# Kernel optimization log

Measured on AMD Instinct MI355X. Metric: run time of the kernel, lower is better.

The kernel has to match this reference:

```python
import jax, jax.numpy as jnp
import numpy as np

N = 50000      # nodes
E = 800000     # edges (avg degree 16)
D_IN = 128     # in_feats
D_H = 128      # n_hidden
D_OUT = 64     # n_classes


def _lin(k, fan_in, fan_out):
    # torch nn.Linear default init: U(-1/sqrt(fan_in), 1/sqrt(fan_in))
    s = 1.0 / np.sqrt(fan_in)
    return jax.random.uniform(k, (fan_in, fan_out), jnp.float32, -s, s)


def setup_inputs() -> dict:
    key = jax.random.key(0)
    ks = jax.random.split(key, 12)
    return {
        "x": jax.random.normal(ks[0], (N, D_IN), jnp.float32),
        "edge_src": jax.random.randint(ks[1], (E,), 0, N, jnp.int32),
        "edge_dst": jax.random.randint(ks[2], (E,), 0, N, jnp.int32),
        # layer 0: in_feats -> n_hidden
        "W_self0": _lin(ks[3], D_IN, D_H),
        "W_neigh0": _lin(ks[4], D_IN, D_H),
        "b0": jnp.zeros((D_H,), jnp.float32),
        # layer 1: n_hidden -> n_hidden
        "W_self1": _lin(ks[5], D_H, D_H),
        "W_neigh1": _lin(ks[6], D_H, D_H),
        "b1": jnp.zeros((D_H,), jnp.float32),
        # layer 2: n_hidden -> n_classes
        "W_self2": _lin(ks[7], D_H, D_OUT),
        "W_neigh2": _lin(ks[8], D_H, D_OUT),
        "b2": jnp.zeros((D_OUT,), jnp.float32),
    }


def _sage_conv(x, src, dst, W_self, W_neigh, b):
    """DGL SAGEConv with 'mean' aggregator:
    out = x @ W_self + mean_{u in N(v)} x_u @ W_neigh + b
    Zero in-degree nodes get zero neighbor term (degree clamped to 1)."""
    n = x.shape[0]
    agg = jax.ops.segment_sum(x[src], dst, num_segments=n)          # [N, d]
    deg = jax.ops.segment_sum(jnp.ones((src.shape[0],), x.dtype), dst,
                              num_segments=n)                        # [N]
    h_neigh = agg / jnp.maximum(deg, 1.0)[:, None]
    return x @ W_self + h_neigh @ W_neigh + b


def reference(x, edge_src, edge_dst,
              W_self0, W_neigh0, b0,
              W_self1, W_neigh1, b1,
              W_self2, W_neigh2, b2):
    # dropout is identity in eval/inference mode
    h = jax.nn.relu(_sage_conv(x, edge_src, edge_dst, W_self0, W_neigh0, b0))
    h = jax.nn.relu(_sage_conv(h, edge_src, edge_dst, W_self1, W_neigh1, b1))
    return _sage_conv(h, edge_src, edge_dst, W_self2, W_neigh2, b2)
```

## Files before the change

kernel.cpp:

```cpp
#include <hip/hip_runtime.h>

#define NN 50000
#define NPAD 50048
#define NE 800000
#define CAP 64
#define NSLICE 6250

#define EBG 391
#define EDGE_BLOCKS (EBG * 8)
#define CVT_BLOCKS 782
#define W_BLOCKS 320
#define PREP_GRID (EDGE_BLOCKS + CVT_BLOCKS + W_BLOCKS)

typedef _Float16 f16;
typedef _Float16 f16x8 __attribute__((ext_vector_type(8)));
typedef float f32x4 __attribute__((ext_vector_type(4)));

__global__ __launch_bounds__(256) void prep_kernel(
    const float* __restrict__ X, const int* __restrict__ esrc,
    const int* __restrict__ edst,
    const float* __restrict__ WS0, const float* __restrict__ WN0,
    const float* __restrict__ WS1, const float* __restrict__ WN1,
    const float* __restrict__ WS2, const float* __restrict__ WN2,
    f16* __restrict__ XH, f16* __restrict__ wt0, f16* __restrict__ wt1,
    f16* __restrict__ wt2, int* __restrict__ cursor, int* __restrict__ eidx) {
    const int bid = blockIdx.x;
    if (bid < EDGE_BLOCKS) {
        const int g = bid & 7;
        const int gi = bid >> 3;
        const int lo = g * NSLICE, hi = lo + NSLICE;
        const int per = (NE + EBG - 1) / EBG;
        const int s = gi * per;
        const int e_end = (s + per < NE) ? s + per : NE;
        for (int e = s + threadIdx.x; e < e_end; e += 256) {
            int d = edst[e];
            if (d >= lo && d < hi) {
                int p = atomicAdd(&cursor[d], 1);
                if (p < CAP) eidx[(d << 6) + p] = esrc[e];
            }
        }
    } else if (bid < EDGE_BLOCKS + CVT_BLOCKS) {
        const int total8 = NN * 128 / 8;
        int t = (bid - EDGE_BLOCKS) * 256 + threadIdx.x;
        for (int i = t; i < total8; i += CVT_BLOCKS * 256) {
            float4 v0 = *reinterpret_cast<const float4*>(X + (size_t)i * 8);
            float4 v1 = *reinterpret_cast<const float4*>(X + (size_t)i * 8 + 4);
            f16x8 o = {(f16)v0.x, (f16)v0.y, (f16)v0.z, (f16)v0.w,
                       (f16)v1.x, (f16)v1.y, (f16)v1.z, (f16)v1.w};
            *reinterpret_cast<f16x8*>(XH + (size_t)i * 8) = o;
        }
    } else {
        int t = (bid - EDGE_BLOCKS - CVT_BLOCKS) * 256 + threadIdx.x;
        if (t < 32768) {
            int j = t >> 8, k = t & 255;
            float v = (k < 128) ? WS0[k * 128 + j] : WN0[(k - 128) * 128 + j];
            wt0[j * 256 + k] = (f16)v;
        } else if (t < 65536) {
            int u = t - 32768;
            int j = u >> 8, k = u & 255;
            float v = (k < 128) ? WS1[k * 128 + j] : WN1[(k - 128) * 128 + j];
            wt1[j * 256 + k] = (f16)v;
        } else if (t < 81920) {
            int u = t - 65536;
            int j = u >> 7, k = u & 127;
            float v = (j < 64) ? WS2[k * 64 + j] : WN2[k * 64 + (j - 64)];
            wt2[j * 128 + k] = (f16)v;
        }
    }
}

__global__ __launch_bounds__(256) void gather_mean4(const f16* __restrict__ X,
                                                    const int* __restrict__ cnt_,
                                                    const int* __restrict__ eidx,
                                                    f16* __restrict__ OUT, int n) {
    int wave = blockIdx.x * 4 + (threadIdx.x >> 6);
    int lane = threadIdx.x & 63;
    int node = wave * 4 + (lane >> 4);
    int sl = lane & 15;
    if (node >= n) return;
    int cnt = cnt_[node];
    const int* row = eidx + ((size_t)node << 6);
    float acc[8];
#pragma unroll
    for (int j = 0; j < 8; j++) acc[j] = 0.f;
    int e = 0;
    for (; e + 8 <= cnt; e += 8) {
        int4 sa = *reinterpret_cast<const int4*>(row + e);
        int4 sb = *reinterpret_cast<const int4*>(row + e + 4);
        f16x8 v0 = *reinterpret_cast<const f16x8*>(X + (size_t)sa.x * 128 + sl * 8);
        f16x8 v1 = *reinterpret_cast<const f16x8*>(X + (size_t)sa.y * 128 + sl * 8);
        f16x8 v2 = *reinterpret_cast<const f16x8*>(X + (size_t)sa.z * 128 + sl * 8);
        f16x8 v3 = *reinterpret_cast<const f16x8*>(X + (size_t)sa.w * 128 + sl * 8);
        f16x8 v4 = *reinterpret_cast<const f16x8*>(X + (size_t)sb.x * 128 + sl * 8);
        f16x8 v5 = *reinterpret_cast<const f16x8*>(X + (size_t)sb.y * 128 + sl * 8);
        f16x8 v6 = *reinterpret_cast<const f16x8*>(X + (size_t)sb.z * 128 + sl * 8);
        f16x8 v7 = *reinterpret_cast<const f16x8*>(X + (size_t)sb.w * 128 + sl * 8);
#pragma unroll
        for (int j = 0; j < 8; j++)
            acc[j] += (((float)v0[j] + (float)v1[j]) + ((float)v2[j] + (float)v3[j])) +
                      (((float)v4[j] + (float)v5[j]) + ((float)v6[j] + (float)v7[j]));
    }
    for (; e + 4 <= cnt; e += 4) {
        int4 s4 = *reinterpret_cast<const int4*>(row + e);
        f16x8 v0 = *reinterpret_cast<const f16x8*>(X + (size_t)s4.x * 128 + sl * 8);
        f16x8 v1 = *reinterpret_cast<const f16x8*>(X + (size_t)s4.y * 128 + sl * 8);
        f16x8 v2 = *reinterpret_cast<const f16x8*>(X + (size_t)s4.z * 128 + sl * 8);
        f16x8 v3 = *reinterpret_cast<const f16x8*>(X + (size_t)s4.w * 128 + sl * 8);
#pragma unroll
        for (int j = 0; j < 8; j++)
            acc[j] += ((float)v0[j] + (float)v1[j]) + ((float)v2[j] + (float)v3[j]);
    }
    for (; e < cnt; e++) {
        int s0 = row[e];
        f16x8 v0 = *reinterpret_cast<const f16x8*>(X + (size_t)s0 * 128 + sl * 8);
#pragma unroll
        for (int j = 0; j < 8; j++) acc[j] += (float)v0[j];
    }
    float iv = 1.0f / fmaxf((float)cnt, 1.0f);
    f16x8 o;
#pragma unroll
    for (int j = 0; j < 8; j++) o[j] = (f16)(acc[j] * iv);
    *reinterpret_cast<f16x8*>(OUT + (size_t)node * 128 + sl * 8) = o;
}

__global__ __launch_bounds__(256) void gather_out(const f16* __restrict__ Y,
                                                  const int* __restrict__ cnt_,
                                                  const int* __restrict__ eidx,
                                                  float* __restrict__ OUT, int n) {
    int wave = blockIdx.x * 4 + (threadIdx.x >> 6);
    int lane = threadIdx.x & 63;
    int node = wave * 8 + (lane >> 3);
    int sl = lane & 7;
    if (node >= n) return;
    int cnt = cnt_[node];
    const int* row = eidx + ((size_t)node << 6);
    float acc[8];
#pragma unroll
    for (int j = 0; j < 8; j++) acc[j] = 0.f;
    int e = 0;
    for (; e + 8 <= cnt; e += 8) {
        int4 sa = *reinterpret_cast<const int4*>(row + e);
        int4 sb = *reinterpret_cast<const int4*>(row + e + 4);
        f16x8 v0 = *reinterpret_cast<const f16x8*>(Y + (size_t)sa.x * 128 + 64 + sl * 8);
        f16x8 v1 = *reinterpret_cast<const f16x8*>(Y + (size_t)sa.y * 128 + 64 + sl * 8);
        f16x8 v2 = *reinterpret_cast<const f16x8*>(Y + (size_t)sa.z * 128 + 64 + sl * 8);
        f16x8 v3 = *reinterpret_cast<const f16x8*>(Y + (size_t)sa.w * 128 + 64 + sl * 8);
        f16x8 v4 = *reinterpret_cast<const f16x8*>(Y + (size_t)sb.x * 128 + 64 + sl * 8);
        f16x8 v5 = *reinterpret_cast<const f16x8*>(Y + (size_t)sb.y * 128 + 64 + sl * 8);
        f16x8 v6 = *reinterpret_cast<const f16x8*>(Y + (size_t)sb.z * 128 + 64 + sl * 8);
        f16x8 v7 = *reinterpret_cast<const f16x8*>(Y + (size_t)sb.w * 128 + 64 + sl * 8);
#pragma unroll
        for (int j = 0; j < 8; j++)
            acc[j] += (((float)v0[j] + (float)v1[j]) + ((float)v2[j] + (float)v3[j])) +
                      (((float)v4[j] + (float)v5[j]) + ((float)v6[j] + (float)v7[j]));
    }
    for (; e + 4 <= cnt; e += 4) {
        int4 s4 = *reinterpret_cast<const int4*>(row + e);
        f16x8 v0 = *reinterpret_cast<const f16x8*>(Y + (size_t)s4.x * 128 + 64 + sl * 8);
        f16x8 v1 = *reinterpret_cast<const f16x8*>(Y + (size_t)s4.y * 128 + 64 + sl * 8);
        f16x8 v2 = *reinterpret_cast<const f16x8*>(Y + (size_t)s4.z * 128 + 64 + sl * 8);
        f16x8 v3 = *reinterpret_cast<const f16x8*>(Y + (size_t)s4.w * 128 + 64 + sl * 8);
#pragma unroll
        for (int j = 0; j < 8; j++)
            acc[j] += ((float)v0[j] + (float)v1[j]) + ((float)v2[j] + (float)v3[j]);
    }
    for (; e < cnt; e++) {
        int s0 = row[e];
        f16x8 v0 = *reinterpret_cast<const f16x8*>(Y + (size_t)s0 * 128 + 64 + sl * 8);
#pragma unroll
        for (int j = 0; j < 8; j++) acc[j] += (float)v0[j];
    }
    float iv = 1.0f / fmaxf((float)cnt, 1.0f);
    f16x8 self = *reinterpret_cast<const f16x8*>(Y + (size_t)node * 128 + sl * 8);
    float o[8];
#pragma unroll
    for (int j = 0; j < 8; j++) o[j] = acc[j] * iv + (float)self[j];
    float* dst = OUT + (size_t)node * 64 + sl * 8;
    *reinterpret_cast<float4*>(dst) = *reinterpret_cast<float4*>(o);
    *reinterpret_cast<float4*>(dst + 4) = *reinterpret_cast<float4*>(o + 4);
}

template <int DOUT, int K, bool RELU, bool HALFBIAS>
__global__ __launch_bounds__(256) void mfma_gemm(const f16* __restrict__ A1,
                                                 const f16* __restrict__ A2,
                                                 const f16* __restrict__ WT,
                                                 const float* __restrict__ BIAS,
                                                 f16* __restrict__ O16, int n) {
    constexpr int MT = 4;
    constexpr int NT = 4;
    const int lane = threadIdx.x & 63;
    const int wid = threadIdx.x >> 6;
    const int m0 = blockIdx.x * 128 + (wid >> 1) * 64;
    const int n0 = (wid & 1) * 64;

    const int ar = lane & 15;
    const int kg = (lane >> 4) * 8;

    f32x4 acc[MT][NT];
#pragma unroll
    for (int mt = 0; mt < MT; mt++)
#pragma unroll
        for (int nt = 0; nt < NT; nt++) acc[mt][nt] = (f32x4){0.f, 0.f, 0.f, 0.f};

#pragma unroll
    for (int k0 = 0; k0 < K; k0 += 32) {
        const f16* Abase = (K == 256 && k0 >= 128) ? A2 : A1;
        const int kk = (k0 & 127) + kg;
        f16x8 a[MT], b[NT];
#pragma unroll
        for (int mt = 0; mt < MT; mt++)
            a[mt] = *reinterpret_cast<const f16x8*>(
                Abase + (size_t)(m0 + mt * 16 + ar) * 128 + kk);
#pragma unroll
        for (int nt = 0; nt < NT; nt++)
            b[nt] = *reinterpret_cast<const f16x8*>(
                WT + (size_t)(n0 + nt * 16 + ar) * K + k0 + kg);
#pragma unroll
        for (int mt = 0; mt < MT; mt++)
#pragma unroll
            for (int nt = 0; nt < NT; nt++)
                acc[mt][nt] = __builtin_amdgcn_mfma_f32_16x16x32_f16(
                    a[mt], b[nt], acc[mt][nt], 0, 0, 0);
    }

    const int orow = (lane >> 4) * 4;
    const int ocol = lane & 15;
#pragma unroll
    for (int nt = 0; nt < NT; nt++) {
        const int col = n0 + nt * 16 + ocol;
        const float bias = HALFBIAS ? (col < 64 ? BIAS[col] : 0.f) : BIAS[col];
#pragma unroll
        for (int mt = 0; mt < MT; mt++) {
#pragma unroll
            for (int j = 0; j < 4; j++) {
                int row = m0 + mt * 16 + orow + j;
                if (row < n) {
                    float v = acc[mt][nt][j] + bias;
                    if (RELU) v = fmaxf(v, 0.f);
                    O16[(size_t)row * DOUT + col] = (f16)v;
                }
            }
        }
    }
}

extern "C" void kernel_launch(void* const* d_in, const int* in_sizes, int n_in,
                              void* d_out, int out_size, void* d_ws, size_t ws_size,
                              hipStream_t stream) {
    const float* x        = (const float*)d_in[0];
    const int*   esrc     = (const int*)d_in[1];
    const int*   edst     = (const int*)d_in[2];
    const float* W_self0  = (const float*)d_in[3];
    const float* W_neigh0 = (const float*)d_in[4];
    const float* b0       = (const float*)d_in[5];
    const float* W_self1  = (const float*)d_in[6];
    const float* W_neigh1 = (const float*)d_in[7];
    const float* b1       = (const float*)d_in[8];
    const float* W_self2  = (const float*)d_in[9];
    const float* W_neigh2 = (const float*)d_in[10];
    const float* b2       = (const float*)d_in[11];
    float* out = (float*)d_out;

    char* ws = (char*)d_ws;
    auto align1k = [](size_t v) { return (v + 1023) & ~(size_t)1023; };
    size_t off = 0;
    int* cursor = (int*)(ws + off); off = align1k(off + (size_t)NN * 4);
    int* eidx   = (int*)(ws + off); off = align1k(off + (size_t)NN * CAP * 4);
    f16* wt0    = (f16*)(ws + off); off = align1k(off + (size_t)128 * 256 * 2);
    f16* wt1    = (f16*)(ws + off); off = align1k(off + (size_t)128 * 256 * 2);
    f16* wt2    = (f16*)(ws + off); off = align1k(off + (size_t)128 * 128 * 2);
    const size_t FEAT16 = (size_t)NPAD * 128 * 2;
    f16* xh = (f16*)(ws + off); off += FEAT16;
    f16* hm = (f16*)(ws + off); off += FEAT16;
    f16* h0 = (f16*)(ws + off); off += FEAT16;
    f16* h1 = (f16*)(ws + off); off += FEAT16;

    const int n = NN;
    const int g4blocks = (n + 15) / 16;
    const int g8blocks = (n + 31) / 32;
    const int gemm_blocks = NPAD / 128;

    hipMemsetAsync(cursor, 0, (size_t)n * sizeof(int), stream);
    prep_kernel<<<PREP_GRID, 256, 0, stream>>>(x, esrc, edst,
                                               W_self0, W_neigh0, W_self1, W_neigh1,
                                               W_self2, W_neigh2,
                                               xh, wt0, wt1, wt2, cursor, eidx);

    gather_mean4<<<g4blocks, 256, 0, stream>>>(xh, cursor, eidx, hm, n);
    mfma_gemm<128, 256, true, false><<<gemm_blocks, 256, 0, stream>>>(xh, hm, wt0, b0,
                                                                      h0, n);
    gather_mean4<<<g4blocks, 256, 0, stream>>>(h0, cursor, eidx, hm, n);
    mfma_gemm<128, 256, true, false><<<gemm_blocks, 256, 0, stream>>>(h0, hm, wt1, b1,
                                                                      h1, n);
    mfma_gemm<128, 128, false, true><<<gemm_blocks, 256, 0, stream>>>(h1, nullptr, wt2,
                                                                      b2, hm, n);
    gather_out<<<g8blocks, 256, 0, stream>>>(hm, cursor, eidx, out, n);
}
```

Before: 194.7 us.

## Fuse neighbor gather with GEMM per layer and shrink edge indices to 16-bit

Each hidden layer now gathers and averages neighbor rows into a swizzled LDS tile, then runs the MFMA GEMM from that tile in the same kernel. This removes the global round trip of the mean buffer and one launch per layer. Edge source indices are stored as u16, halving index traffic, but they only fit because N is 50000, below 65536. The degree clamp to CAP is now explicit, and the fused blocks are only 391 blocks of 512 threads, which may limit gather parallelism.

```diff
diff --git a/kernel.cpp b/kernel.cpp
--- a/kernel.cpp
+++ b/kernel.cpp
@@ -15,6 +15,9 @@
 typedef _Float16 f16;
 typedef _Float16 f16x8 __attribute__((ext_vector_type(8)));
 typedef float f32x4 __attribute__((ext_vector_type(4)));
+typedef unsigned short u16;
+typedef unsigned short u16x4 __attribute__((ext_vector_type(4)));
+typedef unsigned short u16x8 __attribute__((ext_vector_type(8)));
 
 __global__ __launch_bounds__(256) void prep_kernel(
     const float* __restrict__ X, const int* __restrict__ esrc,
@@ -23,7 +26,7 @@
     const float* __restrict__ WS1, const float* __restrict__ WN1,
     const float* __restrict__ WS2, const float* __restrict__ WN2,
     f16* __restrict__ XH, f16* __restrict__ wt0, f16* __restrict__ wt1,
-    f16* __restrict__ wt2, int* __restrict__ cursor, int* __restrict__ eidx) {
+    f16* __restrict__ wt2, int* __restrict__ cursor, u16* __restrict__ eidx) {
     const int bid = blockIdx.x;
     if (bid < EDGE_BLOCKS) {
         const int g = bid & 7;
@@ -36,7 +39,7 @@
             int d = edst[e];
             if (d >= lo && d < hi) {
                 int p = atomicAdd(&cursor[d], 1);
-                if (p < CAP) eidx[(d << 6) + p] = esrc[e];
+                if (p < CAP) eidx[(d << 6) + p] = (u16)esrc[e];
             }
         }
     } else if (bid < EDGE_BLOCKS + CVT_BLOCKS) {
@@ -69,97 +72,226 @@
     }
 }
 
-__global__ __launch_bounds__(256) void gather_mean4(const f16* __restrict__ X,
-                                                    const int* __restrict__ cnt_,
-                                                    const int* __restrict__ eidx,
-                                                    f16* __restrict__ OUT, int n) {
-    int wave = blockIdx.x * 4 + (threadIdx.x >> 6);
-    int lane = threadIdx.x & 63;
-    int node = wave * 4 + (lane >> 4);
-    int sl = lane & 15;
-    if (node >= n) return;
-    int cnt = cnt_[node];
-    const int* row = eidx + ((size_t)node << 6);
-    float acc[8];
-#pragma unroll
-    for (int j = 0; j < 8; j++) acc[j] = 0.f;
-    int e = 0;
-    for (; e + 8 <= cnt; e += 8) {
-        int4 sa = *reinterpret_cast<const int4*>(row + e);
-        int4 sb = *reinterpret_cast<const int4*>(row + e + 4);
-        f16x8 v0 = *reinterpret_cast<const f16x8*>(X + (size_t)sa.x * 128 + sl * 8);
-        f16x8 v1 = *reinterpret_cast<const f16x8*>(X + (size_t)sa.y * 128 + sl * 8);
-        f16x8 v2 = *reinterpret_cast<const f16x8*>(X + (size_t)sa.z * 128 + sl * 8);
-        f16x8 v3 = *reinterpret_cast<const f16x8*>(X + (size_t)sa.w * 128 + sl * 8);
-        f16x8 v4 = *reinterpret_cast<const f16x8*>(X + (size_t)sb.x * 128 + sl * 8);
-        f16x8 v5 = *reinterpret_cast<const f16x8*>(X + (size_t)sb.y * 128 + sl * 8);
-        f16x8 v6 = *reinterpret_cast<const f16x8*>(X + (size_t)sb.z * 128 + sl * 8);
-        f16x8 v7 = *reinterpret_cast<const f16x8*>(X + (size_t)sb.w * 128 + sl * 8);
-#pragma unroll
-        for (int j = 0; j < 8; j++)
-            acc[j] += (((float)v0[j] + (float)v1[j]) + ((float)v2[j] + (float)v3[j])) +
-                      (((float)v4[j] + (float)v5[j]) + ((float)v6[j] + (float)v7[j]));
-    }
-    for (; e + 4 <= cnt; e += 4) {
-        int4 s4 = *reinterpret_cast<const int4*>(row + e);
-        f16x8 v0 = *reinterpret_cast<const f16x8*>(X + (size_t)s4.x * 128 + sl * 8);
-        f16x8 v1 = *reinterpret_cast<const f16x8*>(X + (size_t)s4.y * 128 + sl * 8);
-        f16x8 v2 = *reinterpret_cast<const f16x8*>(X + (size_t)s4.z * 128 + sl * 8);
-        f16x8 v3 = *reinterpret_cast<const f16x8*>(X + (size_t)s4.w * 128 + sl * 8);
-#pragma unroll
-        for (int j = 0; j < 8; j++)
-            acc[j] += ((float)v0[j] + (float)v1[j]) + ((float)v2[j] + (float)v3[j]);
-    }
-    for (; e < cnt; e++) {
-        int s0 = row[e];
-        f16x8 v0 = *reinterpret_cast<const f16x8*>(X + (size_t)s0 * 128 + sl * 8);
-#pragma unroll
-        for (int j = 0; j < 8; j++) acc[j] += (float)v0[j];
-    }
-    float iv = 1.0f / fmaxf((float)cnt, 1.0f);
-    f16x8 o;
-#pragma unroll
-    for (int j = 0; j < 8; j++) o[j] = (f16)(acc[j] * iv);
-    *reinterpret_cast<f16x8*>(OUT + (size_t)node * 128 + sl * 8) = o;
+__global__ __launch_bounds__(512) void fused_layer(const f16* __restrict__ X,
+                                                   const int* __restrict__ cnt_,
+                                                   const u16* __restrict__ eidx,
+                                                   const f16* __restrict__ WT,
+                                                   const float* __restrict__ BIAS,
+                                                   f16* __restrict__ O16, int n) {
+    __shared__ f16 hmt[128 * 128];
+    const int lane = threadIdx.x & 63;
+    const int wid = threadIdx.x >> 6;
+    const int rowbase = blockIdx.x * 128;
+
+    {
+        const int sl = lane & 15;
+#pragma unroll 2
+        for (int it = 0; it < 4; it++) {
+            int nl = wid * 16 + it * 4 + (lane >> 4);
+            int node = rowbase + nl;
+            float acc[8];
+#pragma unroll
+            for (int j = 0; j < 8; j++) acc[j] = 0.f;
+            int cdeg = 0;
+            if (node < n) {
+                cdeg = cnt_[node];
+                int cnt = cdeg < CAP ? cdeg : CAP;
+                const u16* row = eidx + ((size_t)node << 6);
+                int e = 0;
+                for (; e + 8 <= cnt; e += 8) {
+                    u16x8 s8 = *reinterpret_cast<const u16x8*>(row + e);
+                    f16x8 v0 = *reinterpret_cast<const f16x8*>(X + (size_t)s8[0] * 128 + sl * 8);
+                    f16x8 v1 = *reinterpret_cast<const f16x8*>(X + (size_t)s8[1] * 128 + sl * 8);
+                    f16x8 v2 = *reinterpret_cast<const f16x8*>(X + (size_t)s8[2] * 128 + sl * 8);
+                    f16x8 v3 = *reinterpret_cast<const f16x8*>(X + (size_t)s8[3] * 128 + sl * 8);
+                    f16x8 v4 = *reinterpret_cast<const f16x8*>(X + (size_t)s8[4] * 128 + sl * 8);
+                    f16x8 v5 = *reinterpret_cast<const f16x8*>(X + (size_t)s8[5] * 128 + sl * 8);
+                    f16x8 v6 = *reinterpret_cast<const f16x8*>(X + (size_t)s8[6] * 128 + sl * 8);
+                    f16x8 v7 = *reinterpret_cast<const f16x8*>(X + (size_t)s8[7] * 128 + sl * 8);
+#pragma unroll
+                    for (int j = 0; j < 8; j++)
+                        acc[j] += (((float)v0[j] + (float)v1[j]) + ((float)v2[j] + (float)v3[j])) +
+                                  (((float)v4[j] + (float)v5[j]) + ((float)v6[j] + (float)v7[j]));
+                }
+                for (; e + 4 <= cnt; e += 4) {
+                    u16x4 s4 = *reinterpret_cast<const u16x4*>(row + e);
+                    f16x8 v0 = *reinterpret_cast<const f16x8*>(X + (size_t)s4[0] * 128 + sl * 8);
+                    f16x8 v1 = *reinterpret_cast<const f16x8*>(X + (size_t)s4[1] * 128 + sl * 8);
+                    f16x8 v2 = *reinterpret_cast<const f16x8*>(X + (size_t)s4[2] * 128 + sl * 8);
+                    f16x8 v3 = *reinterpret_cast<const f16x8*>(X + (size_t)s4[3] * 128 + sl * 8);
+#pragma unroll
+                    for (int j = 0; j < 8; j++)
+                        acc[j] += ((float)v0[j] + (float)v1[j]) + ((float)v2[j] + (float)v3[j]);
+                }
+                for (; e < cnt; e++) {
+                    int s0 = row[e];
+                    f16x8 v0 = *reinterpret_cast<const f16x8*>(X + (size_t)s0 * 128 + sl * 8);
+#pragma unroll
+                    for (int j = 0; j < 8; j++) acc[j] += (float)v0[j];
+                }
+            }
+            float iv = 1.0f / fmaxf((float)cdeg, 1.0f);
+            f16x8 o;
+#pragma unroll
+            for (int j = 0; j < 8; j++) o[j] = (f16)(acc[j] * iv);
+            int chunk = sl ^ (nl & 7);
+            *reinterpret_cast<f16x8*>(hmt + nl * 128 + chunk * 8) = o;
+        }
+    }
+    __syncthreads();
+
+    constexpr int MT = 4, NT = 2;
+    const int rh = wid >> 2;
+    const int n0 = (wid & 3) * 32;
+    const int ar = lane & 15;
+    const int kq = lane >> 4;
+    const int kg = kq * 8;
+
+    f32x4 acc[MT][NT];
+#pragma unroll
+    for (int mt = 0; mt < MT; mt++)
+#pragma unroll
+        for (int nt = 0; nt < NT; nt++) acc[mt][nt] = (f32x4){0.f, 0.f, 0.f, 0.f};
+
+#pragma unroll
+    for (int k0 = 0; k0 < 256; k0 += 32) {
+        f16x8 a[MT], b[NT];
+#pragma unroll
+        for (int mt = 0; mt < MT; mt++) {
+            const int rl = rh * 64 + mt * 16 + ar;
+            if (k0 < 128) {
+                a[mt] = *reinterpret_cast<const f16x8*>(
+                    X + (size_t)(rowbase + rl) * 128 + k0 + kg);
+            } else {
+                int chunk = ((k0 - 128) >> 3) + kq;
+                a[mt] = *reinterpret_cast<const f16x8*>(
+                    hmt + rl * 128 + (chunk ^ (rl & 7)) * 8);
+            }
+        }
+#pragma unroll
+        for (int nt = 0; nt < NT; nt++)
+            b[nt] = *reinterpret_cast<const f16x8*>(
+                WT + (size_t)(n0 + nt * 16 + ar) * 256 + k0 + kg);
+#pragma unroll
+        for (int mt = 0; mt < MT; mt++)
+#pragma unroll
+            for (int nt = 0; nt < NT; nt++)
+                acc[mt][nt] = __builtin_amdgcn_mfma_f32_16x16x32_f16(
+                    a[mt], b[nt], acc[mt][nt], 0, 0, 0);
+    }
+
+    const int orow = (lane >> 4) * 4;
+    const int ocol = lane & 15;
+#pragma unroll
+    for (int nt = 0; nt < NT; nt++) {
+        const int col = n0 + nt * 16 + ocol;
+        const float bias = BIAS[col];
+#pragma unroll
+        for (int mt = 0; mt < MT; mt++) {
+#pragma unroll
+            for (int j = 0; j < 4; j++) {
+                int row = rowbase + rh * 64 + mt * 16 + orow + j;
+                if (row < n) {
+                    float v = fmaxf(acc[mt][nt][j] + bias, 0.f);
+                    O16[(size_t)row * 128 + col] = (f16)v;
+                }
+            }
+        }
+    }
+}
+
+__global__ __launch_bounds__(256) void gemm2(const f16* __restrict__ A1,
+                                             const f16* __restrict__ WT,
+                                             const float* __restrict__ BIAS,
+                                             f16* __restrict__ O16, int n) {
+    constexpr int MT = 4, NT = 4;
+    const int lane = threadIdx.x & 63;
+    const int wid = threadIdx.x >> 6;
+    const int m0 = blockIdx.x * 128 + (wid >> 1) * 64;
+    const int n0 = (wid & 1) * 64;
+    const int ar = lane & 15;
+    const int kg = (lane >> 4) * 8;
+
+    f32x4 acc[MT][NT];
+#pragma unroll
+    for (int mt = 0; mt < MT; mt++)
+#pragma unroll
+        for (int nt = 0; nt < NT; nt++) acc[mt][nt] = (f32x4){0.f, 0.f, 0.f, 0.f};
+
+#pragma unroll
+    for (int k0 = 0; k0 < 128; k0 += 32) {
+        f16x8 a[MT], b[NT];
+#pragma unroll
+        for (int mt = 0; mt < MT; mt++)
+            a[mt] = *reinterpret_cast<const f16x8*>(
+                A1 + (size_t)(m0 + mt * 16 + ar) * 128 + k0 + kg);
+#pragma unroll
+        for (int nt = 0; nt < NT; nt++)
+            b[nt] = *reinterpret_cast<const f16x8*>(
+                WT + (size_t)(n0 + nt * 16 + ar) * 128 + k0 + kg);
+#pragma unroll
+        for (int mt = 0; mt < MT; mt++)
+#pragma unroll
+            for (int nt = 0; nt < NT; nt++)
+                acc[mt][nt] = __builtin_amdgcn_mfma_f32_16x16x32_f16(
+                    a[mt], b[nt], acc[mt][nt], 0, 0, 0);
+    }
+
+    const int orow = (lane >> 4) * 4;
+    const int ocol = lane & 15;
+#pragma unroll
+    for (int nt = 0; nt < NT; nt++) {
+        const int col = n0 + nt * 16 + ocol;
+        const float bias = (col < 64) ? BIAS[col] : 0.f;
+#pragma unroll
+        for (int mt = 0; mt < MT; mt++) {
+#pragma unroll
+            for (int j = 0; j < 4; j++) {
+                int row = m0 + mt * 16 + orow + j;
+                if (row < n)
+                    O16[(size_t)row * 128 + col] = (f16)(acc[mt][nt][j] + bias);
+            }
+        }
+    }
 }
 
 __global__ __launch_bounds__(256) void gather_out(const f16* __restrict__ Y,
                                                   const int* __restrict__ cnt_,
-                                                  const int* __restrict__ eidx,
+                                                  const u16* __restrict__ eidx,
                                                   float* __restrict__ OUT, int n) {
     int wave = blockIdx.x * 4 + (threadIdx.x >> 6);
     int lane = threadIdx.x & 63;
     int node = wave * 8 + (lane >> 3);
     int sl = lane & 7;
     if (node >= n) return;
-    int cnt = cnt_[node];
-    const int* row = eidx + ((size_t)node << 6);
+    int cdeg = cnt_[node];
+    int cnt = cdeg < CAP ? cdeg : CAP;
+    const u16* row = eidx + ((size_t)node << 6);
     float acc[8];
 #pragma unroll
     for (int j = 0; j < 8; j++) acc[j] = 0.f;
     int e = 0;
     for (; e + 8 <= cnt; e += 8) {
-        int4 sa = *reinterpret_cast<const int4*>(row + e);
-        int4 sb = *reinterpret_cast<const int4*>(row + e + 4);
-        f16x8 v0 = *reinterpret_cast<const f16x8*>(Y + (size_t)sa.x * 128 + 64 + sl * 8);
-        f16x8 v1 = *reinterpret_cast<const f16x8*>(Y + (size_t)sa.y * 128 + 64 + sl * 8);
-        f16x8 v2 = *reinterpret_cast<const f16x8*>(Y + (size_t)sa.z * 128 + 64 + sl * 8);
-        f16x8 v3 = *reinterpret_cast<const f16x8*>(Y + (size_t)sa.w * 128 + 64 + sl * 8);
-        f16x8 v4 = *reinterpret_cast<const f16x8*>(Y + (size_t)sb.x * 128 + 64 + sl * 8);
-        f16x8 v5 = *reinterpret_cast<const f16x8*>(Y + (size_t)sb.y * 128 + 64 + sl * 8);
-        f16x8 v6 = *reinterpret_cast<const f16x8*>(Y + (size_t)sb.z * 128 + 64 + sl * 8);
-        f16x8 v7 = *reinterpret_cast<const f16x8*>(Y + (size_t)sb.w * 128 + 64 + sl * 8);
+        u16x8 s8 = *reinterpret_cast<const u16x8*>(row + e);
+        f16x8 v0 = *reinterpret_cast<const f16x8*>(Y + (size_t)s8[0] * 128 + 64 + sl * 8);
+        f16x8 v1 = *reinterpret_cast<const f16x8*>(Y + (size_t)s8[1] * 128 + 64 + sl * 8);
+        f16x8 v2 = *reinterpret_cast<const f16x8*>(Y + (size_t)s8[2] * 128 + 64 + sl * 8);
+        f16x8 v3 = *reinterpret_cast<const f16x8*>(Y + (size_t)s8[3] * 128 + 64 + sl * 8);
+        f16x8 v4 = *reinterpret_cast<const f16x8*>(Y + (size_t)s8[4] * 128 + 64 + sl * 8);
+        f16x8 v5 = *reinterpret_cast<const f16x8*>(Y + (size_t)s8[5] * 128 + 64 + sl * 8);
+        f16x8 v6 = *reinterpret_cast<const f16x8*>(Y + (size_t)s8[6] * 128 + 64 + sl * 8);
+        f16x8 v7 = *reinterpret_cast<const f16x8*>(Y + (size_t)s8[7] * 128 + 64 + sl * 8);
 #pragma unroll
         for (int j = 0; j < 8; j++)
             acc[j] += (((float)v0[j] + (float)v1[j]) + ((float)v2[j] + (float)v3[j])) +
                       (((float)v4[j] + (float)v5[j]) + ((float)v6[j] + (float)v7[j]));
     }
     for (; e + 4 <= cnt; e += 4) {
-        int4 s4 = *reinterpret_cast<const int4*>(row + e);
-        f16x8 v0 = *reinterpret_cast<const f16x8*>(Y + (size_t)s4.x * 128 + 64 + sl * 8);
-        f16x8 v1 = *reinterpret_cast<const f16x8*>(Y + (size_t)s4.y * 128 + 64 + sl * 8);
-        f16x8 v2 = *reinterpret_cast<const f16x8*>(Y + (size_t)s4.z * 128 + 64 + sl * 8);
-        f16x8 v3 = *reinterpret_cast<const f16x8*>(Y + (size_t)s4.w * 128 + 64 + sl * 8);
+        u16x4 s4 = *reinterpret_cast<const u16x4*>(row + e);
+        f16x8 v0 = *reinterpret_cast<const f16x8*>(Y + (size_t)s4[0] * 128 + 64 + sl * 8);
+        f16x8 v1 = *reinterpret_cast<const f16x8*>(Y + (size_t)s4[1] * 128 + 64 + sl * 8);
+        f16x8 v2 = *reinterpret_cast<const f16x8*>(Y + (size_t)s4[2] * 128 + 64 + sl * 8);
+        f16x8 v3 = *reinterpret_cast<const f16x8*>(Y + (size_t)s4[3] * 128 + 64 + sl * 8);
 #pragma unroll
         for (int j = 0; j < 8; j++)
             acc[j] += ((float)v0[j] + (float)v1[j]) + ((float)v2[j] + (float)v3[j]);
@@ -170,7 +302,7 @@
 #pragma unroll
         for (int j = 0; j < 8; j++) acc[j] += (float)v0[j];
     }
-    float iv = 1.0f / fmaxf((float)cnt, 1.0f);
+    float iv = 1.0f / fmaxf((float)cdeg, 1.0f);
     f16x8 self = *reinterpret_cast<const f16x8*>(Y + (size_t)node * 128 + sl * 8);
     float o[8];
 #pragma unroll
@@ -178,70 +310,6 @@
     float* dst = OUT + (size_t)node * 64 + sl * 8;
     *reinterpret_cast<float4*>(dst) = *reinterpret_cast<float4*>(o);
     *reinterpret_cast<float4*>(dst + 4) = *reinterpret_cast<float4*>(o + 4);
-}
-
-template <int DOUT, int K, bool RELU, bool HALFBIAS>
-__global__ __launch_bounds__(256) void mfma_gemm(const f16* __restrict__ A1,
-                                                 const f16* __restrict__ A2,
-                                                 const f16* __restrict__ WT,
-                                                 const float* __restrict__ BIAS,
-                                                 f16* __restrict__ O16, int n) {
-    constexpr int MT = 4;
-    constexpr int NT = 4;
-    const int lane = threadIdx.x & 63;
-    const int wid = threadIdx.x >> 6;
-    const int m0 = blockIdx.x * 128 + (wid >> 1) * 64;
-    const int n0 = (wid & 1) * 64;
-
-    const int ar = lane & 15;
-    const int kg = (lane >> 4) * 8;
-
-    f32x4 acc[MT][NT];
-#pragma unroll
-    for (int mt = 0; mt < MT; mt++)
-#pragma unroll
-        for (int nt = 0; nt < NT; nt++) acc[mt][nt] = (f32x4){0.f, 0.f, 0.f, 0.f};
-
-#pragma unroll
-    for (int k0 = 0; k0 < K; k0 += 32) {
-        const f16* Abase = (K == 256 && k0 >= 128) ? A2 : A1;
-        const int kk = (k0 & 127) + kg;
-        f16x8 a[MT], b[NT];
-#pragma unroll
-        for (int mt = 0; mt < MT; mt++)
-            a[mt] = *reinterpret_cast<const f16x8*>(
-                Abase + (size_t)(m0 + mt * 16 + ar) * 128 + kk);
-#pragma unroll
-        for (int nt = 0; nt < NT; nt++)
-            b[nt] = *reinterpret_cast<const f16x8*>(
-                WT + (size_t)(n0 + nt * 16 + ar) * K + k0 + kg);
-#pragma unroll
-        for (int mt = 0; mt < MT; mt++)
-#pragma unroll
-            for (int nt = 0; nt < NT; nt++)
-                acc[mt][nt] = __builtin_amdgcn_mfma_f32_16x16x32_f16(
-                    a[mt], b[nt], acc[mt][nt], 0, 0, 0);
-    }
-
-    const int orow = (lane >> 4) * 4;
-    const int ocol = lane & 15;
-#pragma unroll
-    for (int nt = 0; nt < NT; nt++) {
-        const int col = n0 + nt * 16 + ocol;
-        const float bias = HALFBIAS ? (col < 64 ? BIAS[col] : 0.f) : BIAS[col];
-#pragma unroll
-        for (int mt = 0; mt < MT; mt++) {
-#pragma unroll
-            for (int j = 0; j < 4; j++) {
-                int row = m0 + mt * 16 + orow + j;
-                if (row < n) {
-                    float v = acc[mt][nt][j] + bias;
-                    if (RELU) v = fmaxf(v, 0.f);
-                    O16[(size_t)row * DOUT + col] = (f16)v;
-                }
-            }
-        }
-    }
 }
 
 extern "C" void kernel_launch(void* const* d_in, const int* in_sizes, int n_in,
@@ -265,20 +333,19 @@
     auto align1k = [](size_t v) { return (v + 1023) & ~(size_t)1023; };
     size_t off = 0;
     int* cursor = (int*)(ws + off); off = align1k(off + (size_t)NN * 4);
-    int* eidx   = (int*)(ws + off); off = align1k(off + (size_t)NN * CAP * 4);
+    u16* eidx   = (u16*)(ws + off); off = align1k(off + (size_t)NN * CAP * 2);
     f16* wt0    = (f16*)(ws + off); off = align1k(off + (size_t)128 * 256 * 2);
     f16* wt1    = (f16*)(ws + off); off = align1k(off + (size_t)128 * 256 * 2);
     f16* wt2    = (f16*)(ws + off); off = align1k(off + (size_t)128 * 128 * 2);
     const size_t FEAT16 = (size_t)NPAD * 128 * 2;
     f16* xh = (f16*)(ws + off); off += FEAT16;
-    f16* hm = (f16*)(ws + off); off += FEAT16;
     f16* h0 = (f16*)(ws + off); off += FEAT16;
     f16* h1 = (f16*)(ws + off); off += FEAT16;
+    f16* yc = (f16*)(ws + off); off += FEAT16;
 
     const int n = NN;
-    const int g4blocks = (n + 15) / 16;
     const int g8blocks = (n + 31) / 32;
-    const int gemm_blocks = NPAD / 128;
+    const int tile_blocks = NPAD / 128;
 
     hipMemsetAsync(cursor, 0, (size_t)n * sizeof(int), stream);
     prep_kernel<<<PREP_GRID, 256, 0, stream>>>(x, esrc, edst,
@@ -286,13 +353,8 @@
                                                W_self2, W_neigh2,
                                                xh, wt0, wt1, wt2, cursor, eidx);
 
-    gather_mean4<<<g4blocks, 256, 0, stream>>>(xh, cursor, eidx, hm, n);
-    mfma_gemm<128, 256, true, false><<<gemm_blocks, 256, 0, stream>>>(xh, hm, wt0, b0,
-                                                                      h0, n);
-    gather_mean4<<<g4blocks, 256, 0, stream>>>(h0, cursor, eidx, hm, n);
-    mfma_gemm<128, 256, true, false><<<gemm_blocks, 256, 0, stream>>>(h0, hm, wt1, b1,
-                                                                      h1, n);
-    mfma_gemm<128, 128, false, true><<<gemm_blocks, 256, 0, stream>>>(h1, nullptr, wt2,
-                                                                      b2, hm, n);
-    gather_out<<<g8blocks, 256, 0, stream>>>(hm, cursor, eidx, out, n);
-}
+    fused_layer<<<tile_blocks, 512, 0, stream>>>(xh, cursor, eidx, wt0, b0, h0, n);
+    fused_layer<<<tile_blocks, 512, 0, stream>>>(h0, cursor, eidx, wt1, b1, h1, n);
+    gemm2<<<tile_blocks, 256, 0, stream>>>(h1, wt2, b2, yc, n);
+    gather_out<<<g8blocks, 256, 0, stream>>>(yc, cursor, eidx, out, n);
+}
```

Measured after the change: 184.9 us. -5.1%, faster.
